# Kernel optimization log

Hardware: AMD Instinct MI355X
Metric: run time of the kernel (lower is better)

Reference implementation:

```python
import jax, jax.numpy as jnp
import numpy as np

N_HEADS = 4
ITERS = 3
EPS = 1e-8


def layer_norm(x, g, b, eps=1e-5):
    m = jnp.mean(x, axis=-1, keepdims=True)
    v = jnp.mean((x - m) ** 2, axis=-1, keepdims=True)
    return (x - m) * jax.lax.rsqrt(v + eps) * g + b


def gru_cell(x, h, Wih, Whh, bih, bhh):
    # PyTorch GRUCell semantics. x: [M, kvq], h: [M, dim]
    gi = x @ Wih.T + bih
    gh = h @ Whh.T + bhh
    ir, iz, i_n = jnp.split(gi, 3, axis=-1)
    hr, hz, h_n = jnp.split(gh, 3, axis=-1)
    r = jax.nn.sigmoid(ir + hr)
    z = jax.nn.sigmoid(iz + hz)
    n = jnp.tanh(i_n + r * h_n)
    return (1.0 - z) * n + z * h


def slot_attention(features, slots, Wq, Wk, Wv, g_in, b_in, g_s, b_s, Wih, Whh, bih, bhh):
    b, n, _ = features.shape
    _, ns, dim = slots.shape
    kvq = Wk.shape[0]
    dh = kvq // N_HEADS
    scale = dh ** -0.5
    inp = layer_norm(features, g_in, b_in)
    k = (inp @ Wk.T).reshape(b, n, N_HEADS, dh)
    v = (inp @ Wv.T).reshape(b, n, N_HEADS, dh)
    attn_vis = None
    for _ in range(ITERS):
        slots_prev = slots
        s = layer_norm(slots, g_s, b_s)
        q = (s @ Wq.T).reshape(b, ns, N_HEADS, dh)
        dots = jnp.einsum("bihd,bjhd->bihj", q, k) * scale
        attn = jax.nn.softmax(dots, axis=1)  # competitive softmax over slots
        attn_vis = attn.mean(axis=2)  # [b, ns, n]
        w = attn + EPS
        w = w / jnp.sum(w, axis=-1, keepdims=True)  # weighted mean over features
        upd = jnp.einsum("bjhd,bihj->bihd", v, w).reshape(b, ns, kvq)
        slots = gru_cell(upd.reshape(-1, kvq), slots_prev.reshape(-1, dim),
                         Wih, Whh, bih, bhh).reshape(b, ns, dim)
    return slots, attn_vis


def vq_pool(x, codebook):
    # x: [b, ns, d], codebook: [C, d]
    d2 = (jnp.sum(x ** 2, axis=-1, keepdims=True)
          - 2.0 * jnp.einsum("bnd,cd->bnc", x, codebook)
          + jnp.sum(codebook ** 2, axis=-1))
    idx = jnp.argmin(d2, axis=-1)
    q = codebook[idx]
    commit = jnp.mean((x - jax.lax.stop_gradient(q)) ** 2)
    q = x + jax.lax.stop_gradient(q - x)  # straight-through
    return q, idx, commit


def setup_inputs() -> dict:
    key = jax.random.key(0)
    ks = jax.random.split(key, 16)
    B, N, FD = 32, 1024, 768
    NS, D, KVQ, C = 24, 256, 256, 512
    sc = lambda d: d ** -0.5
    return {
        "features": jax.random.normal(ks[0], (B, N, FD), jnp.float32),
        "conditioning": jax.random.normal(ks[1], (B, NS, D), jnp.float32),
        "Wq": jax.random.normal(ks[2], (KVQ, D), jnp.float32) * sc(D),
        "Wk": jax.random.normal(ks[3], (KVQ, FD), jnp.float32) * sc(FD),
        "Wv": jax.random.normal(ks[4], (KVQ, FD), jnp.float32) * sc(FD),
        "g_in": jnp.ones((FD,), jnp.float32),
        "b_in": jnp.zeros((FD,), jnp.float32),
        "g_s": jnp.ones((D,), jnp.float32),
        "b_s": jnp.zeros((D,), jnp.float32),
        "Wih": jax.random.normal(ks[5], (3 * D, KVQ), jnp.float32) * sc(KVQ),
        "Whh": jax.random.normal(ks[6], (3 * D, D), jnp.float32) * sc(D),
        "bih": jnp.zeros((3 * D,), jnp.float32),
        "bhh": jnp.zeros((3 * D,), jnp.float32),
        "codebook": jax.random.normal(ks[7], (C, D), jnp.float32) * sc(D),
    }


def reference(features, conditioning, Wq, Wk, Wv, g_in, b_in, g_s, b_s,
              Wih, Whh, bih, bhh, codebook):
    sa = lambda f, s: slot_attention(f, s, Wq, Wk, Wv, g_in, b_in, g_s, b_s,
                                     Wih, Whh, bih, bhh)
    slots, pre_attn = sa(features, conditioning)
    q_slots, indices, commit = vq_pool(slots, codebook)
    slots, post_attn = sa(features, q_slots)
    return slots, post_attn, pre_attn, indices, commit
```

## Files before the change

kernel.cpp:

```cpp
#include <hip/hip_runtime.h>
#include <math.h>

#define LB __launch_bounds__(256)

constexpr int BATCH = 32, NFEAT = 1024, FDIM = 768, NSLOT = 24;
constexpr int NH = 4, DH = 64, NITER = 3;
constexpr int MF = BATCH * NFEAT;
constexpr int MS = BATCH * NSLOT;
constexpr float QSCALE = 0.125f;
constexpr float ATTN_EPS = 1e-8f;
constexpr float LNEPS = 1e-5f;

typedef __attribute__((ext_vector_type(8))) short bf16x8;
typedef __attribute__((ext_vector_type(4))) float f32x4;

__device__ __forceinline__ unsigned short f2bf(float x) {
  unsigned u = __float_as_uint(x);
  return (unsigned short)((u + 0x7FFFu + ((u >> 16) & 1u)) >> 16);
}
__device__ __forceinline__ float bf2f(unsigned short h) {
  return __uint_as_float(((unsigned)h) << 16);
}
__device__ __forceinline__ void cvt8(const float4& a, const float4& b, float m, float r,
                                     int4& hi, int4& lo) {
  float v[8] = {a.x, a.y, a.z, a.w, b.x, b.y, b.z, b.w};
  unsigned sh[8], sl[8];
#pragma unroll
  for (int j = 0; j < 8; ++j) {
    float vv = (v[j] - m) * r;
    unsigned short h = f2bf(vv);
    sh[j] = h;
    sl[j] = f2bf(vv - bf2f(h));
  }
  hi = make_int4((int)(sh[0] | (sh[1] << 16)), (int)(sh[2] | (sh[3] << 16)),
                 (int)(sh[4] | (sh[5] << 16)), (int)(sh[6] | (sh[7] << 16)));
  lo = make_int4((int)(sl[0] | (sl[1] << 16)), (int)(sl[2] | (sl[3] << 16)),
                 (int)(sl[4] | (sl[5] << 16)), (int)(sl[6] | (sl[7] << 16)));
}

__device__ __forceinline__ void gll16(const void* g, void* l) {
  __builtin_amdgcn_global_load_lds(
      (const __attribute__((address_space(1))) void*)g,
      (__attribute__((address_space(3))) void*)l, 16, 0, 0);
}

__global__ LB void k_preprow(const float* __restrict__ x, float* __restrict__ stats,
                             const float* __restrict__ Wk, const float* __restrict__ Wv,
                             const float* __restrict__ Wq,
                             const float* __restrict__ g_in, const float* __restrict__ b_in,
                             const float* __restrict__ g_s, const float* __restrict__ b_s,
                             short* __restrict__ Bh_g, short* __restrict__ Bl_g,
                             float* __restrict__ Wgq, float* __restrict__ cconst) {
  const int t = threadIdx.x;
  if (blockIdx.x < MF / 4) {
    const int row = blockIdx.x * 4 + (t >> 6);
    const int lane = t & 63;
    const float* xr = x + (size_t)row * FDIM;
    float s = 0.f, sq = 0.f;
#pragma unroll
    for (int i = 0; i < 3; ++i) {
      float4 v = *(const float4*)(xr + i * 256 + lane * 4);
      s += v.x + v.y + v.z + v.w;
      sq += v.x * v.x + v.y * v.y + v.z * v.z + v.w * v.w;
    }
#pragma unroll
    for (int o = 32; o > 0; o >>= 1) { s += __shfl_down(s, o, 64); sq += __shfl_down(sq, o, 64); }
    if (lane == 0) {
      float m = s / (float)FDIM;
      float var = sq / (float)FDIM - m * m;
      stats[row * 2] = m;
      stats[row * 2 + 1] = 1.f / sqrtf(var + LNEPS);
    }
    return;
  }
  const int r = blockIdx.x - MF / 4;
  float s = 0.f;
  if (r < 512) {
    const float* srcW = (r < 256) ? (Wk + (size_t)r * FDIM) : (Wv + (size_t)(r - 256) * FDIM);
    for (int k = t; k < FDIM; k += 256) {
      float w = srcW[k];
      float wg = w * g_in[k];
      s += b_in[k] * w;
      unsigned short h = f2bf(wg);
      Bh_g[(size_t)r * FDIM + k] = (short)h;
      Bl_g[(size_t)r * FDIM + k] = (short)f2bf(wg - bf2f(h));
    }
  } else {
    const int c = r - 512;
    float w = Wq[(size_t)c * 256 + t];
    Wgq[(size_t)c * 256 + t] = w * g_s[t];
    s = b_s[t] * w;
  }
  __shared__ float red[256];
  red[t] = s; __syncthreads();
  for (int o = 128; o > 0; o >>= 1) { if (t < o) red[t] += red[t + o]; __syncthreads(); }
  if (t == 0) cconst[r] = red[0];
}

__global__ LB void k_mfkv(const float* __restrict__ x, const float* __restrict__ stats,
                          const short* __restrict__ Bh_g, const short* __restrict__ Bl_g,
                          const float* __restrict__ cconst,
                          float* __restrict__ kout, float* __restrict__ vout) {
  __shared__ short Ah[2048], Al[2048];
  __shared__ short Bh[2][4096], Bl[2][4096];
  const int t = threadIdx.x;
  const int l = t & 63;
  const int w = t >> 6;
  const int row0 = blockIdx.x * 64;
  const int c0 = blockIdx.y * 128;

  const int sAr = t >> 2;
  const int sl = t & 3;
  const int kqA = sl ^ ((sAr >> 1) & 3);
  const float* pa = x + (size_t)(row0 + sAr) * FDIM + kqA * 8;
  const float mA = stats[(row0 + sAr) * 2], rA = stats[(row0 + sAr) * 2 + 1];
  const int sBr1 = sAr + 64;
  const int kqB1 = sl ^ ((sBr1 >> 1) & 3);
  const short* pkh0 = Bh_g + (size_t)(c0 + sAr) * FDIM + kqA * 8;
  const short* pkh1 = Bh_g + (size_t)(c0 + sBr1) * FDIM + kqB1 * 8;
  const short* pkl0 = Bl_g + (size_t)(c0 + sAr) * FDIM + kqA * 8;
  const short* pkl1 = Bl_g + (size_t)(c0 + sBr1) * FDIM + kqB1 * 8;
  const short* pvh0 = Bh_g + (size_t)(256 + c0 + sAr) * FDIM + kqA * 8;
  const short* pvh1 = Bh_g + (size_t)(256 + c0 + sBr1) * FDIM + kqB1 * 8;
  const short* pvl0 = Bl_g + (size_t)(256 + c0 + sAr) * FDIM + kqA * 8;
  const short* pvl1 = Bl_g + (size_t)(256 + c0 + sBr1) * FDIM + kqB1 * 8;
  const int wbA = t * 16;
  const int wb0 = t * 16, wb1 = (t + 256) * 16;

  const int wm = (w >> 1) * 32, wn = (w & 1) * 64;
  int aoff[2], boff[4];
#pragma unroll
  for (int m = 0; m < 2; ++m) {
    const int ar = wm + m * 16 + (l & 15);
    const int kq = l >> 4;
    aoff[m] = ar * 64 + ((kq ^ ((ar >> 1) & 3)) << 4);
  }
#pragma unroll
  for (int n = 0; n < 4; ++n) {
    const int bc = wn + n * 16 + (l & 15);
    const int kq = l >> 4;
    boff[n] = bc * 64 + ((kq ^ ((bc >> 1) & 3)) << 4);
  }

  f32x4 acc[2][2][4] = {};
  float4 raa = *(const float4*)pa, rab = *(const float4*)(pa + 4);

  for (int s = 0; s < FDIM / 32; ++s) {
    if (s) __syncthreads();
    const int ko = s * 32;
    gll16(pkh0 + ko, (char*)&Bh[0][0] + wb0);
    gll16(pkh1 + ko, (char*)&Bh[0][0] + wb1);
    gll16(pkl0 + ko, (char*)&Bl[0][0] + wb0);
    gll16(pkl1 + ko, (char*)&Bl[0][0] + wb1);
    gll16(pvh0 + ko, (char*)&Bh[1][0] + wb0);
    gll16(pvh1 + ko, (char*)&Bh[1][0] + wb1);
    gll16(pvl0 + ko, (char*)&Bl[1][0] + wb0);
    gll16(pvl1 + ko, (char*)&Bl[1][0] + wb1);
    int4 hi, lo;
    cvt8(raa, rab, mA, rA, hi, lo);
    *(int4*)((char*)Ah + wbA) = hi; *(int4*)((char*)Al + wbA) = lo;
    if (s + 1 < FDIM / 32) {
      raa = *(const float4*)(pa + ko + 32);
      rab = *(const float4*)(pa + ko + 36);
    }
    __syncthreads();
    bf16x8 fah[2], fal[2];
#pragma unroll
    for (int m = 0; m < 2; ++m) {
      fah[m] = *(const bf16x8*)((const char*)Ah + aoff[m]);
      fal[m] = *(const bf16x8*)((const char*)Al + aoff[m]);
    }
#pragma unroll
    for (int kv = 0; kv < 2; ++kv) {
      bf16x8 fbh[4], fbl[4];
#pragma unroll
      for (int n = 0; n < 4; ++n) {
        fbh[n] = *(const bf16x8*)((const char*)&Bh[kv][0] + boff[n]);
        fbl[n] = *(const bf16x8*)((const char*)&Bl[kv][0] + boff[n]);
      }
#pragma unroll
      for (int m = 0; m < 2; ++m)
#pragma unroll
        for (int n = 0; n < 4; ++n) {
          acc[kv][m][n] = __builtin_amdgcn_mfma_f32_16x16x32_bf16(fal[m], fbh[n], acc[kv][m][n], 0, 0, 0);
          acc[kv][m][n] = __builtin_amdgcn_mfma_f32_16x16x32_bf16(fah[m], fbl[n], acc[kv][m][n], 0, 0, 0);
          acc[kv][m][n] = __builtin_amdgcn_mfma_f32_16x16x32_bf16(fah[m], fbh[n], acc[kv][m][n], 0, 0, 0);
        }
    }
  }
#pragma unroll
  for (int kv = 0; kv < 2; ++kv) {
    float* Cout = kv ? vout : kout;
#pragma unroll
    for (int m = 0; m < 2; ++m) {
      const int rbase = row0 + wm + m * 16 + ((l >> 4) << 2);
#pragma unroll
      for (int n = 0; n < 4; ++n) {
        const int col = c0 + wn + n * 16 + (l & 15);
        const float cc = cconst[kv * 256 + col];
#pragma unroll
        for (int r = 0; r < 4; ++r)
          Cout[(size_t)(rbase + r) * 256 + col] = acc[kv][m][n][r] + cc;
      }
    }
  }
}

template <bool WRITE_ATTN>
__global__ LB void k_fdots(const float* __restrict__ slots, const float* __restrict__ Wgq,
                           const float* __restrict__ cconst,
                           const float* __restrict__ kmat, const float* __restrict__ vmat,
                           float* __restrict__ attn, float* __restrict__ updp,
                           float* __restrict__ ssump) {
  const int blk = blockIdx.x;
  const int jc = blk & 3;
  const int h = (blk >> 2) & 3;
  const int b = blk >> 4;
  const int t = threadIdx.x;
  __shared__ float U[NSLOT][256];
  __shared__ float qs[NSLOT][DH];
  __shared__ float vt[DH][DH];
  __shared__ float ssr[NSLOT][8];
  __shared__ float mst[NSLOT], rst[NSLOT];
  if (t < 192) {
    const int r = t >> 3, g = t & 7;
    const float* sr = slots + (size_t)(b * NSLOT + r) * 256 + g * 32;
    float s = 0.f, sq = 0.f;
#pragma unroll
    for (int m4 = 0; m4 < 8; ++m4) {
      float4 v = *(const float4*)(sr + m4 * 4);
      *(float4*)&U[r][g * 32 + m4 * 4] = v;
      s += v.x + v.y + v.z + v.w;
      sq += v.x * v.x + v.y * v.y + v.z * v.z + v.w * v.w;
    }
    s += __shfl_down(s, 4, 8); sq += __shfl_down(sq, 4, 8);
    s += __shfl_down(s, 2, 8); sq += __shfl_down(sq, 2, 8);
    s += __shfl_down(s, 1, 8); sq += __shfl_down(sq, 1, 8);
    if (g == 0) {
      float mm = s * (1.f / 256.f);
      mst[r] = mm;
      rst[r] = 1.f / sqrtf(sq * (1.f / 256.f) - mm * mm + LNEPS);
    }
  }
  __syncthreads();
  for (int lidx = t; lidx < NSLOT * 256; lidx += 256) {
    const int i = lidx >> 8, kk = lidx & 255;
    U[i][kk] = (U[i][kk] - mst[i]) * rst[i];
  }
  __syncthreads();
  {
    const int d = t & 63, ig = t >> 6;
    const float* wrow = Wgq + (size_t)(h * 64 + d) * 256;
    float aq[6] = {};
    for (int k4 = 0; k4 < 256; k4 += 4) {
      const float4 wv = *(const float4*)(wrow + k4);
#pragma unroll
      for (int u = 0; u < 6; ++u) {
        const float4 uv = *(const float4*)&U[ig * 6 + u][k4];
        aq[u] += uv.x * wv.x + uv.y * wv.y + uv.z * wv.z + uv.w * wv.w;
      }
    }
    const float qc = cconst[512 + h * 64 + d];
#pragma unroll
    for (int u = 0; u < 6; ++u) qs[ig * 6 + u][d] = aq[u] + qc;
  }
  __syncthreads();
  const int j = jc * 256 + t;
  const float* kr = kmat + (size_t)(b * NFEAT + j) * 256 + h * 64;
  float acc[NSLOT] = {};
#pragma unroll
  for (int d4 = 0; d4 < DH; d4 += 4) {
    float4 kv = *(const float4*)(kr + d4);
#pragma unroll
    for (int i = 0; i < NSLOT; ++i) {
      float4 qv = *(const float4*)&qs[i][d4];
      acc[i] += qv.x * kv.x + qv.y * kv.y + qv.z * kv.z + qv.w * kv.w;
    }
  }
  float mx = -1e30f;
#pragma unroll
  for (int i = 0; i < NSLOT; ++i) { acc[i] *= QSCALE; mx = fmaxf(mx, acc[i]); }
  float s = 0.f;
#pragma unroll
  for (int i = 0; i < NSLOT; ++i) { acc[i] = expf(acc[i] - mx); s += acc[i]; }
  const float inv = 1.f / s;
  float* ab = attn + (size_t)(b * NH + h) * NSLOT * NFEAT + j;
#pragma unroll
  for (int i = 0; i < NSLOT; ++i) {
    const float wgt = acc[i] * inv;
    if (WRITE_ATTN) ab[(size_t)i * NFEAT] = wgt;
    U[i][t] = wgt + ATTN_EPS;
  }
  __syncthreads();
  if (t < 192) {
    const int i = t >> 3, s8 = t & 7;
    float sp = 0.f;
#pragma unroll
    for (int m = 0; m < 32; ++m) sp += U[i][s8 * 32 + ((m + t) & 31)];
    ssr[i][s8] = sp;
  }
  const int d = t & 63;
  const int ig = t >> 6;
  float acc2[6] = {};
  for (int j0 = 0; j0 < 256; j0 += 64) {
    __syncthreads();
#pragma unroll
    for (int rl = 0; rl < 4; ++rl) {
      const int lidx = rl * 1024 + t * 4;
      const int jj = lidx >> 6, dd = lidx & 63;
      *(float4*)&vt[jj][dd] =
          *(const float4*)(vmat + (size_t)(b * NFEAT + jc * 256 + j0 + jj) * 256 + h * 64 + dd);
    }
    __syncthreads();
#pragma unroll 4
    for (int jj4 = 0; jj4 < 64; jj4 += 4) {
      float4 w4[6];
#pragma unroll
      for (int u = 0; u < 6; ++u) w4[u] = *(const float4*)&U[ig * 6 + u][j0 + jj4];
      const float vv0 = vt[jj4 + 0][d];
      const float vv1 = vt[jj4 + 1][d];
      const float vv2 = vt[jj4 + 2][d];
      const float vv3 = vt[jj4 + 3][d];
#pragma unroll
      for (int u = 0; u < 6; ++u) {
        acc2[u] += w4[u].x * vv0;
        acc2[u] += w4[u].y * vv1;
        acc2[u] += w4[u].z * vv2;
        acc2[u] += w4[u].w * vv3;
      }
    }
  }
  __syncthreads();
  if (t < NSLOT) {
    float sp = 0.f;
#pragma unroll
    for (int u = 0; u < 8; ++u) sp += ssr[t][u];
    ssump[((size_t)(b * NH + h) * 4 + jc) * NSLOT + t] = sp;
  }
  float* up = updp + (((size_t)(b * NH + h) * 4 + jc) * NSLOT) * 64;
#pragma unroll
  for (int u = 0; u < 6; ++u) up[(ig * 6 + u) * 64 + d] = acc2[u];
}

template <bool FINAL>
__global__ LB void k_grufin(const float* __restrict__ updp, const float* __restrict__ ssump,
                            const float* __restrict__ sprev,
                            const float* __restrict__ Wih, const float* __restrict__ Whh,
                            const float* __restrict__ bih, const float* __restrict__ bhh,
                            float* __restrict__ snext, float* __restrict__ outs) {
  __shared__ float updt[8][256];
  __shared__ float Bs[3][16][33];
  const int bx = blockIdx.x;
  const int d0 = blockIdx.y * 32;
  const int rows0 = bx * 8;
  const int t = threadIdx.x;
  {
    const int h = t >> 6, d = t & 63;
#pragma unroll
    for (int u = 0; u < 8; ++u) {
      const int row = rows0 + u;
      const int b = row / 24, i = row - b * 24;
      const size_t base = (size_t)(b * 4 + h) * 4;
      float s = 0.f, wsum = 0.f;
#pragma unroll
      for (int jc = 0; jc < 4; ++jc) {
        s += updp[(base + jc) * (NSLOT * 64) + i * 64 + d];
        wsum += ssump[(base + jc) * NSLOT + i];
      }
      updt[u][h * 64 + d] = s / wsum;
    }
  }
  __syncthreads();
  const int r = t >> 5;
  const int dd = t & 31;
  float accR = 0.f, accZ = 0.f, accN = 0.f, accH = 0.f;
  for (int k0 = 0; k0 < 256; k0 += 16) {
    {
      int i = t;
      {
        const int s = i >> 7, rem = i & 127, c = rem >> 2, kq = rem & 3;
        float4 wv = *(const float4*)(Wih + (size_t)(s * 256 + d0 + c) * 256 + k0 + kq * 4);
        Bs[s][kq * 4 + 0][c] = wv.x; Bs[s][kq * 4 + 1][c] = wv.y;
        Bs[s][kq * 4 + 2][c] = wv.z; Bs[s][kq * 4 + 3][c] = wv.w;
      }
      if (t < 128) {
        i = 256 + t;
        const int s = i >> 7, rem = i & 127, c = rem >> 2, kq = rem & 3;
        float4 wv = *(const float4*)(Wih + (size_t)(s * 256 + d0 + c) * 256 + k0 + kq * 4);
        Bs[s][kq * 4 + 0][c] = wv.x; Bs[s][kq * 4 + 1][c] = wv.y;
        Bs[s][kq * 4 + 2][c] = wv.z; Bs[s][kq * 4 + 3][c] = wv.w;
      }
    }
    __syncthreads();
#pragma unroll
    for (int kk = 0; kk < 16; ++kk) {
      const float a = updt[r][k0 + kk];
      accR += a * Bs[0][kk][dd];
      accZ += a * Bs[1][kk][dd];
      accN += a * Bs[2][kk][dd];
    }
    __syncthreads();
  }
  {
    const int rr2 = t >> 5, c0 = (t & 31) * 8;
    const float* sp = sprev + (size_t)(rows0 + rr2) * 256 + c0;
    *(float4*)&updt[rr2][c0] = *(const float4*)sp;
    *(float4*)&updt[rr2][c0 + 4] = *(const float4*)(sp + 4);
  }
  __syncthreads();
  for (int k0 = 0; k0 < 256; k0 += 16) {
    {
      int i = t;
      {
        const int s = i >> 7, rem = i & 127, c = rem >> 2, kq = rem & 3;
        float4 wv = *(const float4*)(Whh + (size_t)(s * 256 + d0 + c) * 256 + k0 + kq * 4);
        Bs[s][kq * 4 + 0][c] = wv.x; Bs[s][kq * 4 + 1][c] = wv.y;
        Bs[s][kq * 4 + 2][c] = wv.z; Bs[s][kq * 4 + 3][c] = wv.w;
      }
      if (t < 128) {
        i = 256 + t;
        const int s = i >> 7, rem = i & 127, c = rem >> 2, kq = rem & 3;
        float4 wv = *(const float4*)(Whh + (size_t)(s * 256 + d0 + c) * 256 + k0 + kq * 4);
        Bs[s][kq * 4 + 0][c] = wv.x; Bs[s][kq * 4 + 1][c] = wv.y;
        Bs[s][kq * 4 + 2][c] = wv.z; Bs[s][kq * 4 + 3][c] = wv.w;
      }
    }
    __syncthreads();
#pragma unroll
    for (int kk = 0; kk < 16; ++kk) {
      const float a = updt[r][k0 + kk];
      accR += a * Bs[0][kk][dd];
      accZ += a * Bs[1][kk][dd];
      accH += a * Bs[2][kk][dd];
    }
    __syncthreads();
  }
  const int row = rows0 + r;
  const int c = d0 + dd;
  const float hp = updt[r][c];
  const float rr = 1.f / (1.f + expf(-(accR + bih[c] + bhh[c])));
  const float zz = 1.f / (1.f + expf(-(accZ + bih[256 + c] + bhh[256 + c])));
  const float nn = tanhf(accN + bih[512 + c] + rr * (accH + bhh[512 + c]));
  const float o = (1.f - zz) * nn + zz * hp;
  snext[(size_t)row * 256 + c] = o;
  if (FINAL) outs[(size_t)row * 256 + c] = o;
}

__global__ LB void k_attnvis(const float* __restrict__ attn, float* __restrict__ out) {
  const int idx = blockIdx.x * 256 + threadIdx.x;
  const int j = idx & 1023;
  const int rem = idx >> 10;
  const int i = rem % NSLOT;
  const int b = rem / NSLOT;
  float s = 0.f;
#pragma unroll
  for (int h = 0; h < NH; ++h)
    s += attn[(size_t)((b * NH + h) * NSLOT + i) * NFEAT + j];
  out[idx] = 0.25f * s;
}

__global__ LB void k_vqvis(float* __restrict__ slots, const float* __restrict__ cb,
                           const float* __restrict__ attn,
                           float* __restrict__ idx_out, float* __restrict__ bestd2,
                           float* __restrict__ vis_out) {
  const int t = threadIdx.x;
  if (blockIdx.x >= MS) {
    const int idx = (blockIdx.x - MS) * 256 + t;
    const int j = idx & 1023;
    const int rem = idx >> 10;
    const int i = rem % NSLOT;
    const int b = rem / NSLOT;
    float s = 0.f;
#pragma unroll
    for (int h = 0; h < NH; ++h)
      s += attn[(size_t)((b * NH + h) * NSLOT + i) * NFEAT + j];
    vis_out[idx] = 0.25f * s;
    return;
  }
  const int r = blockIdx.x;
  __shared__ float xs[256];
  __shared__ float red[256];
  __shared__ float rv[256];
  __shared__ int ri[256];
  xs[t] = slots[(size_t)r * 256 + t];
  __syncthreads();
  red[t] = xs[t] * xs[t]; __syncthreads();
  for (int o = 128; o > 0; o >>= 1) { if (t < o) red[t] += red[t + o]; __syncthreads(); }
  const float x2 = red[0];
  float best = 1e30f; int bidx = 0;
#pragma unroll
  for (int cset = 0; cset < 2; ++cset) {
    const int c = cset * 256 + t;
    const float* cr = cb + (size_t)c * 256;
    float xc = 0.f, cc = 0.f;
    for (int dd = 0; dd < 256; dd += 4) {
      float4 cv = *(const float4*)(cr + dd);
      xc += xs[dd] * cv.x + xs[dd + 1] * cv.y + xs[dd + 2] * cv.z + xs[dd + 3] * cv.w;
      cc += cv.x * cv.x + cv.y * cv.y + cv.z * cv.z + cv.w * cv.w;
    }
    float d2 = x2 - 2.f * xc + cc;
    if (d2 < best) { best = d2; bidx = c; }
  }
  rv[t] = best; ri[t] = bidx; __syncthreads();
  for (int o = 128; o > 0; o >>= 1) {
    if (t < o) {
      if (rv[t + o] < rv[t] || (rv[t + o] == rv[t] && ri[t + o] < ri[t])) {
        rv[t] = rv[t + o]; ri[t] = ri[t + o];
      }
    }
    __syncthreads();
  }
  const int wi = ri[0];
  const float cval = cb[(size_t)wi * 256 + t];
  const float diff = xs[t] - cval;
  red[t] = diff * diff; __syncthreads();
  for (int o = 128; o > 0; o >>= 1) { if (t < o) red[t] += red[t + o]; __syncthreads(); }
  if (t == 0) { idx_out[r] = (float)wi; bestd2[r] = red[0]; }
  slots[(size_t)r * 256 + t] = cval;
}

__global__ LB void k_commit(const float* __restrict__ bestd2, float* __restrict__ out) {
  const int t = threadIdx.x;
  __shared__ float red[256];
  float s = 0.f;
  for (int i = t; i < MS; i += 256) s += bestd2[i];
  red[t] = s; __syncthreads();
  for (int o = 128; o > 0; o >>= 1) { if (t < o) red[t] += red[t + o]; __syncthreads(); }
  if (t == 0) out[0] = red[0] / (float)(MS * 256);
}

extern "C" void kernel_launch(void* const* d_in, const int* in_sizes, int n_in,
                              void* d_out, int out_size, void* d_ws, size_t ws_size,
                              hipStream_t stream) {
  const float* features = (const float*)d_in[0];
  const float* cond = (const float*)d_in[1];
  const float* Wq = (const float*)d_in[2];
  const float* Wk = (const float*)d_in[3];
  const float* Wv = (const float*)d_in[4];
  const float* g_in = (const float*)d_in[5];
  const float* b_in = (const float*)d_in[6];
  const float* g_s = (const float*)d_in[7];
  const float* b_s = (const float*)d_in[8];
  const float* Wih = (const float*)d_in[9];
  const float* Whh = (const float*)d_in[10];
  const float* bih = (const float*)d_in[11];
  const float* bhh = (const float*)d_in[12];
  const float* cb = (const float*)d_in[13];
  float* out = (float*)d_out;

  char* wsb = (char*)d_ws;
  short* Bh_g = (short*)wsb; wsb += (size_t)512 * FDIM * 2;
  short* Bl_g = (short*)wsb; wsb += (size_t)512 * FDIM * 2;
  float* ws = (float*)wsb;
  float* stats = ws;  ws += 2 * MF;
  float* kbuf = ws;   ws += (size_t)MF * 256;
  float* vbuf = ws;   ws += (size_t)MF * 256;
  float* attn = ws;   ws += (size_t)BATCH * NH * NSLOT * NFEAT;
  float* sbufA = ws;  ws += (size_t)MS * 256;
  float* sbufB = ws;  ws += (size_t)MS * 256;
  float* updp = ws;   ws += (size_t)512 * NSLOT * 64;
  float* ssump = ws;  ws += (size_t)512 * NSLOT;
  float* Wgq = ws;    ws += 256 * 256;
  float* cconst = ws; ws += 768;
  float* bestd2 = ws; ws += MS;

  float* out_slots = out;
  float* out_post = out + 196608;
  float* out_pre = out + 196608 + 786432;
  float* out_idx = out + 196608 + 786432 * 2;
  float* out_commit = out_idx + 768;

  k_preprow<<<MF / 4 + 768, 256, 0, stream>>>(features, stats, Wk, Wv, Wq, g_in, b_in,
                                              g_s, b_s, Bh_g, Bl_g, Wgq, cconst);
  k_mfkv<<<dim3(MF / 64, 2), 256, 0, stream>>>(features, stats, Bh_g, Bl_g, cconst, kbuf, vbuf);

  const float* scur = cond;
  float* bufs[2] = {sbufA, sbufB};
  int nb = 0;
  for (int call = 0; call < 2; ++call) {
    for (int it = 0; it < NITER; ++it) {
      float* snxt = bufs[nb]; nb ^= 1;
      if (it == NITER - 1)
        k_fdots<true><<<512, 256, 0, stream>>>(scur, Wgq, cconst, kbuf, vbuf, attn, updp, ssump);
      else
        k_fdots<false><<<512, 256, 0, stream>>>(scur, Wgq, cconst, kbuf, vbuf, attn, updp, ssump);
      if (call == 1 && it == NITER - 1)
        k_grufin<true><<<dim3(MS / 8, 8), 256, 0, stream>>>(updp, ssump, scur, Wih, Whh,
                                                            bih, bhh, snxt, out_slots);
      else
        k_grufin<false><<<dim3(MS / 8, 8), 256, 0, stream>>>(updp, ssump, scur, Wih, Whh,
                                                             bih, bhh, snxt, out_slots);
      scur = snxt;
    }
    if (call == 0) {
      k_vqvis<<<MS + BATCH * NSLOT * NFEAT / 256, 256, 0, stream>>>(
          (float*)scur, cb, attn, out_idx, bestd2, out_pre);
      k_commit<<<1, 256, 0, stream>>>(bestd2, out_commit);
    } else {
      k_attnvis<<<BATCH * NSLOT * NFEAT / 256, 256, 0, stream>>>(attn, out_post);
    }
  }
}
```

Baseline: 659.0 us.

## Compute slot-key dot products with split-bf16 MFMA instead of scalar FP32

The K projection is now stored as hi/lo bf16 pairs, and k_fdots computes the q·k scores with three-pass split-bf16 MFMA on a swizzled, zero-padded 32-row q tile in shared memory. The scalar FP32 dot loop with 24 accumulators per thread is removed, and the score tile goes through shared memory before the softmax. Storage per K element stays at 4 bytes, so global traffic is about the same. The cost is an extra shared-memory round trip for the scores, padding work on 8 unused slot rows, and slightly different rounding.

```diff
diff --git a/kernel.cpp b/kernel.cpp
--- a/kernel.cpp
+++ b/kernel.cpp
@@ -100,7 +100,8 @@
 __global__ LB void k_mfkv(const float* __restrict__ x, const float* __restrict__ stats,
                           const short* __restrict__ Bh_g, const short* __restrict__ Bl_g,
                           const float* __restrict__ cconst,
-                          float* __restrict__ kout, float* __restrict__ vout) {
+                          short* __restrict__ khi, short* __restrict__ klo,
+                          float* __restrict__ vout) {
   __shared__ short Ah[2048], Al[2048];
   __shared__ short Bh[2][4096], Bl[2][4096];
   const int t = threadIdx.x;
@@ -189,18 +190,20 @@
     }
   }
 #pragma unroll
-  for (int kv = 0; kv < 2; ++kv) {
-    float* Cout = kv ? vout : kout;
-#pragma unroll
-    for (int m = 0; m < 2; ++m) {
-      const int rbase = row0 + wm + m * 16 + ((l >> 4) << 2);
-#pragma unroll
-      for (int n = 0; n < 4; ++n) {
-        const int col = c0 + wn + n * 16 + (l & 15);
-        const float cc = cconst[kv * 256 + col];
-#pragma unroll
-        for (int r = 0; r < 4; ++r)
-          Cout[(size_t)(rbase + r) * 256 + col] = acc[kv][m][n][r] + cc;
+  for (int m = 0; m < 2; ++m) {
+    const int rbase = row0 + wm + m * 16 + ((l >> 4) << 2);
+#pragma unroll
+    for (int n = 0; n < 4; ++n) {
+      const int col = c0 + wn + n * 16 + (l & 15);
+      const float cck = cconst[col];
+      const float ccv = cconst[256 + col];
+#pragma unroll
+      for (int r = 0; r < 4; ++r) {
+        const float kval = acc[0][m][n][r] + cck;
+        const unsigned short h = f2bf(kval);
+        khi[(size_t)(rbase + r) * 256 + col] = (short)h;
+        klo[(size_t)(rbase + r) * 256 + col] = (short)f2bf(kval - bf2f(h));
+        vout[(size_t)(rbase + r) * 256 + col] = acc[1][m][n][r] + ccv;
       }
     }
   }
@@ -209,7 +212,8 @@
 template <bool WRITE_ATTN>
 __global__ LB void k_fdots(const float* __restrict__ slots, const float* __restrict__ Wgq,
                            const float* __restrict__ cconst,
-                           const float* __restrict__ kmat, const float* __restrict__ vmat,
+                           const short* __restrict__ khi, const short* __restrict__ klo,
+                           const float* __restrict__ vmat,
                            float* __restrict__ attn, float* __restrict__ updp,
                            float* __restrict__ ssump) {
   const int blk = blockIdx.x;
@@ -217,8 +221,10 @@
   const int h = (blk >> 2) & 3;
   const int b = blk >> 4;
   const int t = threadIdx.x;
-  __shared__ float U[NSLOT][256];
-  __shared__ float qs[NSLOT][DH];
+  const int l = t & 63;
+  const int w = t >> 6;
+  __shared__ float Uat[32 * 256];
+  __shared__ short qh[2048], ql[2048];
   __shared__ float vt[DH][DH];
   __shared__ float ssr[NSLOT][8];
   __shared__ float mst[NSLOT], rst[NSLOT];
@@ -229,7 +235,7 @@
 #pragma unroll
     for (int m4 = 0; m4 < 8; ++m4) {
       float4 v = *(const float4*)(sr + m4 * 4);
-      *(float4*)&U[r][g * 32 + m4 * 4] = v;
+      *(float4*)&Uat[r * 256 + g * 32 + m4 * 4] = v;
       s += v.x + v.y + v.z + v.w;
       sq += v.x * v.x + v.y * v.y + v.z * v.z + v.w * v.w;
     }
@@ -245,7 +251,7 @@
   __syncthreads();
   for (int lidx = t; lidx < NSLOT * 256; lidx += 256) {
     const int i = lidx >> 8, kk = lidx & 255;
-    U[i][kk] = (U[i][kk] - mst[i]) * rst[i];
+    Uat[i * 256 + kk] = (Uat[i * 256 + kk] - mst[i]) * rst[i];
   }
   __syncthreads();
   {
@@ -256,47 +262,97 @@
       const float4 wv = *(const float4*)(wrow + k4);
 #pragma unroll
       for (int u = 0; u < 6; ++u) {
-        const float4 uv = *(const float4*)&U[ig * 6 + u][k4];
+        const float4 uv = *(const float4*)&Uat[(ig * 6 + u) * 256 + k4];
         aq[u] += uv.x * wv.x + uv.y * wv.y + uv.z * wv.z + uv.w * wv.w;
       }
     }
     const float qc = cconst[512 + h * 64 + d];
 #pragma unroll
-    for (int u = 0; u < 6; ++u) qs[ig * 6 + u][d] = aq[u] + qc;
-  }
-  __syncthreads();
-  const int j = jc * 256 + t;
-  const float* kr = kmat + (size_t)(b * NFEAT + j) * 256 + h * 64;
-  float acc[NSLOT] = {};
-#pragma unroll
-  for (int d4 = 0; d4 < DH; d4 += 4) {
-    float4 kv = *(const float4*)(kr + d4);
+    for (int u = 0; u < 6; ++u) {
+      const int row = ig * 6 + u;
+      const float qv = aq[u] + qc;
+      const unsigned short hh = f2bf(qv);
+      const unsigned short ll2 = f2bf(qv - bf2f(hh));
+      const int slot = row * 8 + ((d >> 3) ^ (row & 7));
+      qh[slot * 8 + (d & 7)] = (short)hh;
+      ql[slot * 8 + (d & 7)] = (short)ll2;
+    }
+#pragma unroll
+    for (int z = 0; z < 2; ++z) {
+      const int e = z * 256 + t;
+      const int row = 24 + (e >> 6), dd = e & 63;
+      const int slot = row * 8 + ((dd >> 3) ^ (row & 7));
+      qh[slot * 8 + (dd & 7)] = 0;
+      ql[slot * 8 + (dd & 7)] = 0;
+    }
+  }
+  __syncthreads();
+  {
+    const short* khb = khi + (size_t)(b * NFEAT + jc * 256) * 256 + h * 64;
+    const short* klb = klo + (size_t)(b * NFEAT + jc * 256) * 256 + h * 64;
+    f32x4 scc[2][4] = {};
+#pragma unroll
+    for (int ks = 0; ks < 2; ++ks) {
+      bf16x8 ah[2], al[2];
+#pragma unroll
+      for (int m = 0; m < 2; ++m) {
+        const int row = m * 16 + (l & 15);
+        const int g = ks * 4 + (l >> 4);
+        const int slot = row * 8 + (g ^ (row & 7));
+        ah[m] = *(const bf16x8*)&qh[slot * 8];
+        al[m] = *(const bf16x8*)&ql[slot * 8];
+      }
+#pragma unroll
+      for (int nl = 0; nl < 4; ++nl) {
+        const int nt = w * 4 + nl;
+        const size_t boffg = (size_t)(nt * 16 + (l & 15)) * 256 + ks * 32 + (l >> 4) * 8;
+        const bf16x8 bh = *(const bf16x8*)(khb + boffg);
+        const bf16x8 bl2 = *(const bf16x8*)(klb + boffg);
+#pragma unroll
+        for (int m = 0; m < 2; ++m) {
+          scc[m][nl] = __builtin_amdgcn_mfma_f32_16x16x32_bf16(al[m], bh, scc[m][nl], 0, 0, 0);
+          scc[m][nl] = __builtin_amdgcn_mfma_f32_16x16x32_bf16(ah[m], bl2, scc[m][nl], 0, 0, 0);
+          scc[m][nl] = __builtin_amdgcn_mfma_f32_16x16x32_bf16(ah[m], bh, scc[m][nl], 0, 0, 0);
+        }
+      }
+    }
+#pragma unroll
+    for (int m = 0; m < 2; ++m)
+#pragma unroll
+      for (int nl = 0; nl < 4; ++nl) {
+        const int col = (w * 4 + nl) * 16 + (l & 15);
+        const int rbase = m * 16 + ((l >> 4) << 2);
+#pragma unroll
+        for (int r = 0; r < 4; ++r)
+          Uat[(rbase + r) * 256 + col] = scc[m][nl][r];
+      }
+  }
+  __syncthreads();
+  {
+    float acc[NSLOT];
+#pragma unroll
+    for (int i = 0; i < NSLOT; ++i) acc[i] = Uat[i * 256 + t];
+    float mx = -1e30f;
+#pragma unroll
+    for (int i = 0; i < NSLOT; ++i) { acc[i] *= QSCALE; mx = fmaxf(mx, acc[i]); }
+    float s = 0.f;
+#pragma unroll
+    for (int i = 0; i < NSLOT; ++i) { acc[i] = expf(acc[i] - mx); s += acc[i]; }
+    const float inv = 1.f / s;
+    float* ab = attn + (size_t)(b * NH + h) * NSLOT * NFEAT + jc * 256 + t;
 #pragma unroll
     for (int i = 0; i < NSLOT; ++i) {
-      float4 qv = *(const float4*)&qs[i][d4];
-      acc[i] += qv.x * kv.x + qv.y * kv.y + qv.z * kv.z + qv.w * kv.w;
-    }
-  }
-  float mx = -1e30f;
-#pragma unroll
-  for (int i = 0; i < NSLOT; ++i) { acc[i] *= QSCALE; mx = fmaxf(mx, acc[i]); }
-  float s = 0.f;
-#pragma unroll
-  for (int i = 0; i < NSLOT; ++i) { acc[i] = expf(acc[i] - mx); s += acc[i]; }
-  const float inv = 1.f / s;
-  float* ab = attn + (size_t)(b * NH + h) * NSLOT * NFEAT + j;
-#pragma unroll
-  for (int i = 0; i < NSLOT; ++i) {
-    const float wgt = acc[i] * inv;
-    if (WRITE_ATTN) ab[(size_t)i * NFEAT] = wgt;
-    U[i][t] = wgt + ATTN_EPS;
+      const float wgt = acc[i] * inv;
+      if (WRITE_ATTN) ab[(size_t)i * NFEAT] = wgt;
+      Uat[i * 256 + t] = wgt + ATTN_EPS;
+    }
   }
   __syncthreads();
   if (t < 192) {
     const int i = t >> 3, s8 = t & 7;
     float sp = 0.f;
 #pragma unroll
-    for (int m = 0; m < 32; ++m) sp += U[i][s8 * 32 + ((m + t) & 31)];
+    for (int m = 0; m < 32; ++m) sp += Uat[i * 256 + s8 * 32 + ((m + t) & 31)];
     ssr[i][s8] = sp;
   }
   const int d = t & 63;
@@ -316,7 +372,7 @@
     for (int jj4 = 0; jj4 < 64; jj4 += 4) {
       float4 w4[6];
 #pragma unroll
-      for (int u = 0; u < 6; ++u) w4[u] = *(const float4*)&U[ig * 6 + u][j0 + jj4];
+      for (int u = 0; u < 6; ++u) w4[u] = *(const float4*)&Uat[(ig * 6 + u) * 256 + j0 + jj4];
       const float vv0 = vt[jj4 + 0][d];
       const float vv1 = vt[jj4 + 1][d];
       const float vv2 = vt[jj4 + 2][d];
@@ -551,9 +607,10 @@
   char* wsb = (char*)d_ws;
   short* Bh_g = (short*)wsb; wsb += (size_t)512 * FDIM * 2;
   short* Bl_g = (short*)wsb; wsb += (size_t)512 * FDIM * 2;
+  short* khi = (short*)wsb; wsb += (size_t)MF * 256 * 2;
+  short* klo = (short*)wsb; wsb += (size_t)MF * 256 * 2;
   float* ws = (float*)wsb;
   float* stats = ws;  ws += 2 * MF;
-  float* kbuf = ws;   ws += (size_t)MF * 256;
   float* vbuf = ws;   ws += (size_t)MF * 256;
   float* attn = ws;   ws += (size_t)BATCH * NH * NSLOT * NFEAT;
   float* sbufA = ws;  ws += (size_t)MS * 256;
@@ -572,7 +629,8 @@
 
   k_preprow<<<MF / 4 + 768, 256, 0, stream>>>(features, stats, Wk, Wv, Wq, g_in, b_in,
                                               g_s, b_s, Bh_g, Bl_g, Wgq, cconst);
-  k_mfkv<<<dim3(MF / 64, 2), 256, 0, stream>>>(features, stats, Bh_g, Bl_g, cconst, kbuf, vbuf);
+  k_mfkv<<<dim3(MF / 64, 2), 256, 0, stream>>>(features, stats, Bh_g, Bl_g, cconst,
+                                               khi, klo, vbuf);
 
   const float* scur = cond;
   float* bufs[2] = {sbufA, sbufB};
@@ -581,9 +639,11 @@
     for (int it = 0; it < NITER; ++it) {
       float* snxt = bufs[nb]; nb ^= 1;
       if (it == NITER - 1)
-        k_fdots<true><<<512, 256, 0, stream>>>(scur, Wgq, cconst, kbuf, vbuf, attn, updp, ssump);
+        k_fdots<true><<<512, 256, 0, stream>>>(scur, Wgq, cconst, khi, klo, vbuf,
+                                               attn, updp, ssump);
       else
-        k_fdots<false><<<512, 256, 0, stream>>>(scur, Wgq, cconst, kbuf, vbuf, attn, updp, ssump);
+        k_fdots<false><<<512, 256, 0, stream>>>(scur, Wgq, cconst, khi, klo, vbuf,
+                                                attn, updp, ssump);
       if (call == 1 && it == NITER - 1)
         k_grufin<true><<<dim3(MS / 8, 8), 256, 0, stream>>>(updp, ssump, scur, Wih, Whh,
                                                             bih, bhh, snxt, out_slots);
```

Measured after the change: 642.3 us. 2.5% less time.
